# Kernel optimization log

Hardware: AMD Instinct MI355X
Metric: run time of the kernel (lower is better)

## Reference

```python
import jax, jax.numpy as jnp
import numpy as np

NEG_SLOPE = 0.2

def _leaky_relu(x):
    return jnp.where(x >= 0, x, NEG_SLOPE * x)

def setup_inputs() -> dict:
    key = jax.random.key(0)
    k1, k2, k3 = jax.random.split(key, 3)
    N, E, D = 100000, 3200000, 128
    h = jax.random.normal(k1, (N, D), dtype=jnp.float32)
    g = jax.random.randint(k2, (E, 2), 0, N)          # edge list (src, dst)
    W = jax.random.normal(k3, (1, 2 * D), dtype=jnp.float32) * 0.05  # attnn weight
    b = jnp.zeros((1,), dtype=jnp.float32)            # attnn bias
    return {"g": g, "h": h, "i": 0, "j": 1, "W": W, "b": b}

def reference(g, h, i, j, W, b):
    # e(u, v) = leakyrelu( a^T [h_u || h_v] + b ).
    # Split the linear over the concat: a^T[h_u||h_v] = h_u @ W1^T + h_v @ W2^T,
    # so per-node projections replace a per-edge [E, 2D] concat.
    D = h.shape[1]
    W1, W2 = W[:, :D], W[:, D:]
    s_src = (h @ W1.T)[:, 0]   # [N] contribution as source
    s_dst = (h @ W2.T)[:, 0]   # [N] contribution as destination
    e = _leaky_relu(s_src[g[:, 0]] + s_dst[g[:, 1]] + b[0])  # [E] edge scores
    sumneighbors = jnp.sum(jnp.where(g[:, 0] == i, e, jnp.float32(0)))
    e_ij = _leaky_relu(s_src[i] + s_dst[j] + b[0])
    return jnp.reshape(e_ij / sumneighbors, (1,))
```

## Files before the change

### kernel.cpp

```cpp
#include <hip/hip_runtime.h>

#define D 128
#define NEG_SLOPE 0.2f

__device__ __forceinline__ float leaky(float x) {
    return (x >= 0.0f) ? x : NEG_SLOPE * x;
}

__global__ void precompute_kernel(const float* __restrict__ h,
                                  const float* __restrict__ W,
                                  const int* __restrict__ ip,
                                  const int* __restrict__ jp,
                                  float* __restrict__ ws) {
    int lane = threadIdx.x;
    int iv = ip[0];
    int jv = jp[0];
    float a = h[(long long)iv * D + lane]       * W[lane]
            + h[(long long)iv * D + lane + 64]  * W[lane + 64];
    float c = h[(long long)jv * D + lane]       * W[D + lane]
            + h[(long long)jv * D + lane + 64]  * W[D + lane + 64];
    #pragma unroll
    for (int off = 32; off > 0; off >>= 1) {
        a += __shfl_down(a, off);
        c += __shfl_down(c, off);
    }
    if (lane == 0) {
        ws[0] = 0.0f;
        ws[1] = a;
        ws[2] = c;
    }
}

__global__ void scan_edges_kernel(const int4* __restrict__ g2,
                                  long long npairs,
                                  const int* __restrict__ gtail,
                                  long long E,
                                  const float* __restrict__ h,
                                  const float* __restrict__ W,
                                  const int* __restrict__ ip,
                                  const float* __restrict__ bptr,
                                  float* __restrict__ ws) {
    long long idx = (long long)blockIdx.x * blockDim.x + threadIdx.x;
    int iv = ip[0];

    int src0 = -1, dst0 = 0, src1 = -1, dst1 = 0;
    if (idx < npairs) {
        int4 e = g2[idx];
        src0 = e.x; dst0 = e.y;
        src1 = e.z; dst1 = e.w;
    } else if (idx == npairs && (E & 1)) {
        src0 = gtail[2 * (E - 1)];
        dst0 = gtail[2 * (E - 1) + 1];
    }

    bool m0 = (src0 == iv);
    bool m1 = (src1 == iv);
    if (!(m0 || m1)) return;

    float sSrc = ws[1];
    float b0 = bptr[0];
    const float4* w2 = (const float4*)(W + D);
    float acc = 0.0f;

    if (m0) {
        const float4* hr = (const float4*)(h + (long long)dst0 * D);
        float dot = 0.0f;
        #pragma unroll
        for (int q = 0; q < D / 4; ++q) {
            float4 hv = hr[q];
            float4 wv = w2[q];
            dot += hv.x * wv.x + hv.y * wv.y + hv.z * wv.z + hv.w * wv.w;
        }
        acc += leaky(sSrc + dot + b0);
    }
    if (m1) {
        const float4* hr = (const float4*)(h + (long long)dst1 * D);
        float dot = 0.0f;
        #pragma unroll
        for (int q = 0; q < D / 4; ++q) {
            float4 hv = hr[q];
            float4 wv = w2[q];
            dot += hv.x * wv.x + hv.y * wv.y + hv.z * wv.z + hv.w * wv.w;
        }
        acc += leaky(sSrc + dot + b0);
    }
    atomicAdd(ws, acc);
}

__global__ void finalize_kernel(const float* __restrict__ bptr,
                                const float* __restrict__ ws,
                                float* __restrict__ out) {
    float e_ij = leaky(ws[1] + ws[2] + bptr[0]);
    out[0] = e_ij / ws[0];
}

extern "C" void kernel_launch(void* const* d_in, const int* in_sizes, int n_in,
                              void* d_out, int out_size, void* d_ws, size_t ws_size,
                              hipStream_t stream) {
    const int*   g = (const int*)d_in[0];
    const float* h = (const float*)d_in[1];
    const int*   ip = (const int*)d_in[2];
    const int*   jp = (const int*)d_in[3];
    const float* W = (const float*)d_in[4];
    const float* b = (const float*)d_in[5];
    float* out = (float*)d_out;
    float* ws = (float*)d_ws;

    long long E = (long long)in_sizes[0] / 2;
    long long npairs = E / 2;
    long long nthreads = npairs + (E & 1);
    int block = 256;
    long long grid = (nthreads + block - 1) / block;

    precompute_kernel<<<1, 64, 0, stream>>>(h, W, ip, jp, ws);
    scan_edges_kernel<<<(int)grid, block, 0, stream>>>(
        (const int4*)g, npairs, g, E, h, W, ip, b, ws);
    finalize_kernel<<<1, 1, 0, stream>>>(b, ws, out);
}
```

Measured before the change: 106.4 us.

## Fuse precompute, edge scan and finalize into one kernel with last-block reduction

Merges the three kernels into one launch. Matching threads now compute the source projection inline, and the final block, detected through an atomic counter, computes e_ij and writes the output. A memset replaces the precompute kernel's zeroing of the workspace. This removes two kernel launches and their serialization, but every block now pays for a __syncthreads and an atomic counter increment, plus a threadfence on matching threads.

```diff
diff --git a/kernel.cpp b/kernel.cpp
--- a/kernel.cpp
+++ b/kernel.cpp
@@ -7,39 +7,21 @@
     return (x >= 0.0f) ? x : NEG_SLOPE * x;
 }
 
-__global__ void precompute_kernel(const float* __restrict__ h,
-                                  const float* __restrict__ W,
-                                  const int* __restrict__ ip,
-                                  const int* __restrict__ jp,
-                                  float* __restrict__ ws) {
-    int lane = threadIdx.x;
-    int iv = ip[0];
-    int jv = jp[0];
-    float a = h[(long long)iv * D + lane]       * W[lane]
-            + h[(long long)iv * D + lane + 64]  * W[lane + 64];
-    float c = h[(long long)jv * D + lane]       * W[D + lane]
-            + h[(long long)jv * D + lane + 64]  * W[D + lane + 64];
-    #pragma unroll
-    for (int off = 32; off > 0; off >>= 1) {
-        a += __shfl_down(a, off);
-        c += __shfl_down(c, off);
-    }
-    if (lane == 0) {
-        ws[0] = 0.0f;
-        ws[1] = a;
-        ws[2] = c;
-    }
-}
+__global__ void __launch_bounds__(256)
+gat_scan_finalize(const int4* __restrict__ g2,
+                  long long npairs,
+                  const int* __restrict__ gtail,
+                  long long E,
+                  const float* __restrict__ h,
+                  const float* __restrict__ W,
+                  const int* __restrict__ ip,
+                  const int* __restrict__ jp,
+                  const float* __restrict__ bptr,
+                  float* __restrict__ ws,
+                  float* __restrict__ out) {
+    __shared__ bool amLast;
+    __shared__ float s_sum;
 
-__global__ void scan_edges_kernel(const int4* __restrict__ g2,
-                                  long long npairs,
-                                  const int* __restrict__ gtail,
-                                  long long E,
-                                  const float* __restrict__ h,
-                                  const float* __restrict__ W,
-                                  const int* __restrict__ ip,
-                                  const float* __restrict__ bptr,
-                                  float* __restrict__ ws) {
     long long idx = (long long)blockIdx.x * blockDim.x + threadIdx.x;
     int iv = ip[0];
 
@@ -55,43 +37,75 @@
 
     bool m0 = (src0 == iv);
     bool m1 = (src1 == iv);
-    if (!(m0 || m1)) return;
 
-    float sSrc = ws[1];
-    float b0 = bptr[0];
-    const float4* w2 = (const float4*)(W + D);
-    float acc = 0.0f;
+    if (m0 || m1) {
+        float b0 = bptr[0];
+        const float4* w1 = (const float4*)W;
+        const float4* w2 = (const float4*)(W + D);
 
-    if (m0) {
-        const float4* hr = (const float4*)(h + (long long)dst0 * D);
-        float dot = 0.0f;
-        #pragma unroll
+        const float4* hi = (const float4*)(h + (long long)iv * D);
+        float sSrc = 0.0f;
+        #pragma unroll 8
         for (int q = 0; q < D / 4; ++q) {
-            float4 hv = hr[q];
-            float4 wv = w2[q];
-            dot += hv.x * wv.x + hv.y * wv.y + hv.z * wv.z + hv.w * wv.w;
+            float4 hv = hi[q];
+            float4 wv = w1[q];
+            sSrc += hv.x * wv.x + hv.y * wv.y + hv.z * wv.z + hv.w * wv.w;
         }
-        acc += leaky(sSrc + dot + b0);
+
+        float acc = 0.0f;
+        if (m0) {
+            const float4* hr = (const float4*)(h + (long long)dst0 * D);
+            float dot = 0.0f;
+            #pragma unroll 8
+            for (int q = 0; q < D / 4; ++q) {
+                float4 hv = hr[q];
+                float4 wv = w2[q];
+                dot += hv.x * wv.x + hv.y * wv.y + hv.z * wv.z + hv.w * wv.w;
+            }
+            acc += leaky(sSrc + dot + b0);
+        }
+        if (m1) {
+            const float4* hr = (const float4*)(h + (long long)dst1 * D);
+            float dot = 0.0f;
+            #pragma unroll 8
+            for (int q = 0; q < D / 4; ++q) {
+                float4 hv = hr[q];
+                float4 wv = w2[q];
+                dot += hv.x * wv.x + hv.y * wv.y + hv.z * wv.z + hv.w * wv.w;
+            }
+            acc += leaky(sSrc + dot + b0);
+        }
+        atomicAdd(&ws[0], acc);
+        __threadfence();
     }
-    if (m1) {
-        const float4* hr = (const float4*)(h + (long long)dst1 * D);
-        float dot = 0.0f;
-        #pragma unroll
-        for (int q = 0; q < D / 4; ++q) {
-            float4 hv = hr[q];
-            float4 wv = w2[q];
-            dot += hv.x * wv.x + hv.y * wv.y + hv.z * wv.z + hv.w * wv.w;
+
+    __syncthreads();
+    if (threadIdx.x == 0) {
+        unsigned int old = atomicAdd((unsigned int*)&ws[1], 1u);
+        amLast = (old == gridDim.x - 1);
+    }
+    __syncthreads();
+
+    if (amLast) {
+        if (threadIdx.x == 0) {
+            s_sum = atomicAdd(&ws[0], 0.0f);
         }
-        acc += leaky(sSrc + dot + b0);
+        __syncthreads();
+        int lane = threadIdx.x;
+        if (lane < 64) {
+            int jv = jp[0];
+            float b0 = bptr[0];
+            float a = h[(long long)iv * D + lane]      * W[lane]
+                    + h[(long long)iv * D + lane + 64] * W[lane + 64]
+                    + h[(long long)jv * D + lane]      * W[D + lane]
+                    + h[(long long)jv * D + lane + 64] * W[D + lane + 64];
+            #pragma unroll
+            for (int off = 32; off > 0; off >>= 1)
+                a += __shfl_down(a, off);
+            if (lane == 0)
+                out[0] = leaky(a + b0) / s_sum;
+        }
     }
-    atomicAdd(ws, acc);
-}
-
-__global__ void finalize_kernel(const float* __restrict__ bptr,
-                                const float* __restrict__ ws,
-                                float* __restrict__ out) {
-    float e_ij = leaky(ws[1] + ws[2] + bptr[0]);
-    out[0] = e_ij / ws[0];
 }
 
 extern "C" void kernel_launch(void* const* d_in, const int* in_sizes, int n_in,
@@ -112,8 +126,7 @@
     int block = 256;
     long long grid = (nthreads + block - 1) / block;
 
-    precompute_kernel<<<1, 64, 0, stream>>>(h, W, ip, jp, ws);
-    scan_edges_kernel<<<(int)grid, block, 0, stream>>>(
-        (const int4*)g, npairs, g, E, h, W, ip, b, ws);
-    finalize_kernel<<<1, 1, 0, stream>>>(b, ws, out);
+    hipMemsetAsync(d_ws, 0, 2 * sizeof(float), stream);
+    gat_scan_finalize<<<(int)grid, block, 0, stream>>>(
+        (const int4*)g, npairs, g, E, h, W, ip, jp, b, ws, out);
 }
```

After: 173.2 us. +62.7%, slower.
